# Kernel tuning notes

Measured on AMD Instinct MI355X. Metric: run time of the kernel, lower is better.

## Reference

```python
import jax, jax.numpy as jnp
import numpy as np

N_WIRES = 5
TOTAL = 2 * N_WIRES          # query branch simulates 2*n_wires qubits
DIM = 1 << TOTAL             # 1024
ENC = 1 << N_WIRES           # 32 = token encoder output dim


def setup_inputs() -> dict:
    key = jax.random.key(0)
    ks = jax.random.split(key, 6)
    B, T, C = 4, 32, 512
    x = jax.random.normal(ks[0], (B, T, C), jnp.float32)
    W_tok = jax.random.normal(ks[1], (ENC, C), jnp.float32) * 0.05
    b_tok = jax.random.normal(ks[2], (ENC,), jnp.float32) * 0.05
    theta_rx0 = jax.random.normal(ks[3], (TOTAL,), jnp.float32)
    theta_ry0 = jax.random.normal(ks[4], (TOTAL,), jnp.float32)
    theta_ry1 = jax.random.normal(ks[5], (TOTAL,), jnp.float32)
    return {"x": x, "W_tok": W_tok, "b_tok": b_tok,
            "theta_rx0": theta_rx0, "theta_ry0": theta_ry0, "theta_ry1": theta_ry1}


def _rx_mat(t):
    c = jnp.cos(t / 2).astype(jnp.complex64)
    s = jnp.sin(t / 2).astype(jnp.complex64)
    return jnp.stack([jnp.stack([c, -1j * s]), jnp.stack([-1j * s, c])])


def _ry_mat(t):
    c = jnp.cos(t / 2).astype(jnp.complex64)
    s = jnp.sin(t / 2).astype(jnp.complex64)
    return jnp.stack([jnp.stack([c, -s]), jnp.stack([s, c])])


def _apply_1q(state, U, w):
    # state: (bsz, 2, 2, ..., 2); wire w lives on axis 1+w (wire 0 = MSB)
    s = jnp.tensordot(state, U, axes=((1 + w,), (1,)))  # gate axis moves to last
    return jnp.moveaxis(s, -1, 1 + w)


def _apply_cnot(state, c, t):
    s = jnp.moveaxis(state, (1 + c, 1 + t), (-2, -1))
    s = s.at[..., 1, :].set(s[..., 1, ::-1])  # flip target where control == 1
    return jnp.moveaxis(s, (-2, -1), (1 + c, 1 + t))


def reference(x, W_tok, b_tok, theta_rx0, theta_ry0, theta_ry1):
    B, T, C = x.shape
    # token encoding + L2 normalize  -> (B, T, 32)
    enc = x @ W_tok.T + b_tok
    enc = enc / jnp.linalg.norm(enc, axis=-1, keepdims=True)
    # all T*T pairwise outer products, flattened as a_idx*32 + b_idx  -> (B, T*T, 1024)
    pairs = jnp.einsum('bip,bjq->bijpq', enc, enc).reshape(B, T * T, DIM)
    pairs = pairs / jnp.linalg.norm(pairs, axis=-1, keepdims=True)
    state = pairs.astype(jnp.complex64).reshape((B * T * T,) + (2,) * TOTAL)
    # layer 1: RX then RY on every wire
    for j in range(TOTAL):
        state = _apply_1q(state, _rx_mat(theta_rx0[j]), j)
        state = _apply_1q(state, _ry_mat(theta_ry0[j]), j)
    # CNOT ring
    for j in range(TOTAL):
        state = _apply_cnot(state, j, (j + 1) % TOTAL)
    # layer 2: RY on every wire
    for j in range(TOTAL):
        state = _apply_1q(state, _ry_mat(theta_ry1[j]), j)
    return state.reshape(B, T * T, DIM)
```

## Files before the change

### kernel.cpp

```cpp
#include <hip/hip_runtime.h>
#include <hip/hip_bf16.h>


__device__ __forceinline__ float2 shflx(float2 v, int mask) {
    return make_float2(__shfl_xor(v.x, mask, 64), __shfl_xor(v.y, mask, 64));
}

__global__ __launch_bounds__(256) void fused_kernel(const float* __restrict__ x,
                                                    const float* __restrict__ W,
                                                    const float* __restrict__ bt,
                                                    const float* __restrict__ rx0,
                                                    const float* __restrict__ ry0,
                                                    const float* __restrict__ ry1,
                                                    float* __restrict__ out,
                                                    int complex_out) {
    int bx = blockIdx.x;
    int b  = bx >> 8;
    int i  = (bx >> 3) & 31;
    int j0 = (bx & 7) * 4;
    int tid = threadIdx.x;

    __shared__ float g1[10][8];
    __shared__ float g2[10][2];
    __shared__ float esum[5][32];
    __shared__ float e[5][32];
    __shared__ float2 su[128];
    __shared__ float2 sv[4][128];

    if (tid < 10) {
        float sx, cx, s0, c0, s1, c1;
        sincosf(rx0[tid] * 0.5f, &sx, &cx);
        sincosf(ry0[tid] * 0.5f, &s0, &c0);
        sincosf(ry1[tid] * 0.5f, &s1, &c1);
        g1[tid][0] = c0 * cx;  g1[tid][1] = s0 * sx;
        g1[tid][2] = -s0 * cx; g1[tid][3] = -c0 * sx;
        g1[tid][4] = s0 * cx;  g1[tid][5] = -c0 * sx;
        g1[tid][6] = c0 * cx;  g1[tid][7] = -s0 * sx;
        g2[tid][0] = c1;       g2[tid][1] = s1;
    }

    {
        int col = tid >> 3;
        int kk  = tid & 7;
        const float4* wp = (const float4*)(W + (size_t)col * 512 + kk * 4);
        const float4* xp[5];
        xp[0] = (const float4*)(x + (size_t)(b * 32 + i) * 512 + kk * 4);
#pragma unroll
        for (int v = 1; v < 5; ++v)
            xp[v] = (const float4*)(x + (size_t)(b * 32 + j0 + v - 1) * 512 + kk * 4);
        float acc[5] = {0.f, 0.f, 0.f, 0.f, 0.f};
#pragma unroll
        for (int m = 0; m < 16; ++m) {
            float4 wv = wp[m * 8];
#pragma unroll
            for (int v = 0; v < 5; ++v) {
                float4 xv = xp[v][m * 8];
                acc[v] += xv.x * wv.x + xv.y * wv.y + xv.z * wv.z + xv.w * wv.w;
            }
        }
#pragma unroll
        for (int v = 0; v < 5; ++v) {
            acc[v] += __shfl_xor(acc[v], 1, 64);
            acc[v] += __shfl_xor(acc[v], 2, 64);
            acc[v] += __shfl_xor(acc[v], 4, 64);
        }
        if (kk == 0) {
#pragma unroll
            for (int v = 0; v < 5; ++v) esum[v][col] = acc[v];
        }
    }
    __syncthreads();

    if (tid < 160) {
        int v = tid >> 5, col = tid & 31;
        float sum = esum[v][col] + bt[col];
        float sq = sum * sum;
#pragma unroll
        for (int off = 1; off < 32; off <<= 1) sq += __shfl_xor(sq, off, 64);
        e[v][col] = sum * (1.0f / sqrtf(sq));
    }
    __syncthreads();

    {
        int grp = tid >> 5;
        int p = tid & 31;
#pragma unroll
        for (int it = 0; it < 3; ++it) {
            int job = it * 8 + grp;
            if (job < 20) {
                int v = job >> 2;
                int br = job & 3;
                int s = br >> 1, t = br & 1;
                int side = (v == 0) ? 0 : 1;
                int wb = side * 5;
                float2 c = make_float2(e[v][p], 0.f);
#pragma unroll
                for (int l = 0; l < 5; ++l) {
                    int w = wb + l, bit = 1 << (4 - l);
                    float2 pr = shflx(c, bit);
                    float a0 = g1[w][0], a1 = g1[w][1], a2 = g1[w][2], a3 = g1[w][3];
                    float a4 = g1[w][4], a5 = g1[w][5], a6 = g1[w][6], a7 = g1[w][7];
                    float2 lo, hi;
                    lo.x = a0 * c.x - a1 * c.y + a2 * pr.x - a3 * pr.y;
                    lo.y = a0 * c.y + a1 * c.x + a2 * pr.y + a3 * pr.x;
                    hi.x = a4 * pr.x - a5 * pr.y + a6 * c.x - a7 * c.y;
                    hi.y = a4 * pr.y + a5 * pr.x + a6 * c.y + a7 * c.x;
                    c = ((p & bit) == 0) ? lo : hi;
                }
                if (side == 0) {
#pragma unroll
                    for (int l = 0; l < 4; ++l) {
                        int cb = 1 << (4 - l), tb = 1 << (3 - l);
                        float2 pr = shflx(c, tb);
                        if (p & cb) c = pr;
                    }
                    if ((p & 1) != s) c = make_float2(0.f, 0.f);
                    { float2 pr = shflx(c, 16); if (t) c = pr; }
                } else {
                    { float2 pr = shflx(c, 16); if (s) c = pr; }
#pragma unroll
                    for (int l = 0; l < 4; ++l) {
                        int cb = 1 << (4 - l), tb = 1 << (3 - l);
                        float2 pr = shflx(c, tb);
                        if (p & cb) c = pr;
                    }
                    if ((p & 1) != t) c = make_float2(0.f, 0.f);
                }
#pragma unroll
                for (int l = 0; l < 5; ++l) {
                    int w = wb + l, bit = 1 << (4 - l);
                    float cy = g2[w][0], sy = g2[w][1];
                    float2 pr = shflx(c, bit);
                    c = ((p & bit) == 0)
                          ? make_float2(cy * c.x - sy * pr.x, cy * c.y - sy * pr.y)
                          : make_float2(sy * pr.x + cy * c.x, sy * pr.y + cy * c.y);
                }
                if (v == 0) su[br * 32 + p] = c;
                else        sv[v - 1][br * 32 + p] = c;
            }
        }
    }
    __syncthreads();

    int d0 = tid << 2;
    int pp = d0 >> 5;
    int q0 = d0 & 31;
    float2 up0 = su[pp], up1 = su[32 + pp], up2 = su[64 + pp], up3 = su[96 + pp];

#pragma unroll
    for (int jj = 0; jj < 4; ++jj) {
        const float2* svj = sv[jj];
        float2 acc[4];
#pragma unroll
        for (int ee = 0; ee < 4; ++ee) {
            int q = q0 + ee;
            float2 v0 = svj[q], v1 = svj[32 + q], v2 = svj[64 + q], v3 = svj[96 + q];
            float2 a;
            a.x = up0.x * v0.x - up0.y * v0.y + up1.x * v1.x - up1.y * v1.y
                + up2.x * v2.x - up2.y * v2.y + up3.x * v3.x - up3.y * v3.y;
            a.y = up0.x * v0.y + up0.y * v0.x + up1.x * v1.y + up1.y * v1.x
                + up2.x * v2.y + up2.y * v2.x + up3.x * v3.y + up3.y * v3.x;
            acc[ee] = a;
        }
        size_t pair = (size_t)b * 1024 + (size_t)i * 32 + (j0 + jj);
        if (complex_out) {
            float4* o = (float4*)(out + (pair * 1024 + d0) * 2);
            o[0] = make_float4(acc[0].x, acc[0].y, acc[1].x, acc[1].y);
            o[1] = make_float4(acc[2].x, acc[2].y, acc[3].x, acc[3].y);
        } else {
            float4* o = (float4*)(out + pair * 1024 + d0);
            o[0] = make_float4(acc[0].x, acc[1].x, acc[2].x, acc[3].x);
        }
    }
}

extern "C" void kernel_launch(void* const* d_in, const int* in_sizes, int n_in,
                              void* d_out, int out_size, void* d_ws, size_t ws_size,
                              hipStream_t stream) {
    const float* x   = (const float*)d_in[0];
    const float* W   = (const float*)d_in[1];
    const float* bt  = (const float*)d_in[2];
    const float* rx0 = (const float*)d_in[3];
    const float* ry0 = (const float*)d_in[4];
    const float* ry1 = (const float*)d_in[5];

    int complex_out = (out_size > 4 * 1024 * 1024) ? 1 : 0;
    fused_kernel<<<1024, 256, 0, stream>>>(x, W, bt, rx0, ry0, ry1,
                                           (float*)d_out, complex_out);
}
```

Before: 84.59 us.

## Split token encoding and per-token circuit into prep kernel, add nontemporal output stores

Moves the token encoder GEMV, normalization and the per-half circuit transforms into a separate prep kernel that runs once per token row (128 blocks). It writes U/V factor vectors to workspace, and the outer-product kernel then only loads them and writes the output. Before, each of the 1024 blocks recomputed five encodings and twenty circuit jobs, so this removes redundant compute. It also switches output writes to nontemporal stores. The cost is an extra kernel launch and a workspace round trip.

```diff
diff --git a/kernel.cpp b/kernel.cpp
--- a/kernel.cpp
+++ b/kernel.cpp
@@ -1,31 +1,28 @@
 #include <hip/hip_runtime.h>
 #include <hip/hip_bf16.h>
 
+
+typedef float vfloat4 __attribute__((ext_vector_type(4)));
 
 __device__ __forceinline__ float2 shflx(float2 v, int mask) {
     return make_float2(__shfl_xor(v.x, mask, 64), __shfl_xor(v.y, mask, 64));
 }
 
-__global__ __launch_bounds__(256) void fused_kernel(const float* __restrict__ x,
-                                                    const float* __restrict__ W,
-                                                    const float* __restrict__ bt,
-                                                    const float* __restrict__ rx0,
-                                                    const float* __restrict__ ry0,
-                                                    const float* __restrict__ ry1,
-                                                    float* __restrict__ out,
-                                                    int complex_out) {
-    int bx = blockIdx.x;
-    int b  = bx >> 8;
-    int i  = (bx >> 3) & 31;
-    int j0 = (bx & 7) * 4;
+__global__ __launch_bounds__(256) void prep_kernel(const float* __restrict__ x,
+                                                   const float* __restrict__ W,
+                                                   const float* __restrict__ bt,
+                                                   const float* __restrict__ rx0,
+                                                   const float* __restrict__ ry0,
+                                                   const float* __restrict__ ry1,
+                                                   float2* __restrict__ U,
+                                                   float2* __restrict__ V) {
+    int row = blockIdx.x;
     int tid = threadIdx.x;
 
     __shared__ float g1[10][8];
     __shared__ float g2[10][2];
-    __shared__ float esum[5][32];
-    __shared__ float e[5][32];
-    __shared__ float2 su[128];
-    __shared__ float2 sv[4][128];
+    __shared__ float esum[32];
+    __shared__ float e[32];
 
     if (tid < 10) {
         float sx, cx, s0, c0, s1, c1;
@@ -43,103 +40,100 @@
         int col = tid >> 3;
         int kk  = tid & 7;
         const float4* wp = (const float4*)(W + (size_t)col * 512 + kk * 4);
-        const float4* xp[5];
-        xp[0] = (const float4*)(x + (size_t)(b * 32 + i) * 512 + kk * 4);
-#pragma unroll
-        for (int v = 1; v < 5; ++v)
-            xp[v] = (const float4*)(x + (size_t)(b * 32 + j0 + v - 1) * 512 + kk * 4);
-        float acc[5] = {0.f, 0.f, 0.f, 0.f, 0.f};
+        const float4* xp = (const float4*)(x + (size_t)row * 512 + kk * 4);
+        float acc = 0.f;
 #pragma unroll
         for (int m = 0; m < 16; ++m) {
             float4 wv = wp[m * 8];
-#pragma unroll
-            for (int v = 0; v < 5; ++v) {
-                float4 xv = xp[v][m * 8];
-                acc[v] += xv.x * wv.x + xv.y * wv.y + xv.z * wv.z + xv.w * wv.w;
-            }
+            float4 xv = xp[m * 8];
+            acc += xv.x * wv.x + xv.y * wv.y + xv.z * wv.z + xv.w * wv.w;
         }
-#pragma unroll
-        for (int v = 0; v < 5; ++v) {
-            acc[v] += __shfl_xor(acc[v], 1, 64);
-            acc[v] += __shfl_xor(acc[v], 2, 64);
-            acc[v] += __shfl_xor(acc[v], 4, 64);
-        }
-        if (kk == 0) {
-#pragma unroll
-            for (int v = 0; v < 5; ++v) esum[v][col] = acc[v];
-        }
+        acc += __shfl_xor(acc, 1, 64);
+        acc += __shfl_xor(acc, 2, 64);
+        acc += __shfl_xor(acc, 4, 64);
+        if (kk == 0) esum[col] = acc;
     }
     __syncthreads();
 
-    if (tid < 160) {
-        int v = tid >> 5, col = tid & 31;
-        float sum = esum[v][col] + bt[col];
+    if (tid < 32) {
+        float sum = esum[tid] + bt[tid];
         float sq = sum * sum;
 #pragma unroll
         for (int off = 1; off < 32; off <<= 1) sq += __shfl_xor(sq, off, 64);
-        e[v][col] = sum * (1.0f / sqrtf(sq));
+        e[tid] = sum * (1.0f / sqrtf(sq));
     }
     __syncthreads();
 
     {
         int grp = tid >> 5;
+        int side = grp >> 2;
+        int br = grp & 3;
+        int s = br >> 1, t = br & 1;
         int p = tid & 31;
+        int wb = side * 5;
+        float2 c = make_float2(e[p], 0.f);
 #pragma unroll
-        for (int it = 0; it < 3; ++it) {
-            int job = it * 8 + grp;
-            if (job < 20) {
-                int v = job >> 2;
-                int br = job & 3;
-                int s = br >> 1, t = br & 1;
-                int side = (v == 0) ? 0 : 1;
-                int wb = side * 5;
-                float2 c = make_float2(e[v][p], 0.f);
+        for (int l = 0; l < 5; ++l) {
+            int w = wb + l, bit = 1 << (4 - l);
+            float2 pr = shflx(c, bit);
+            float a0 = g1[w][0], a1 = g1[w][1], a2 = g1[w][2], a3 = g1[w][3];
+            float a4 = g1[w][4], a5 = g1[w][5], a6 = g1[w][6], a7 = g1[w][7];
+            float2 lo, hi;
+            lo.x = a0 * c.x - a1 * c.y + a2 * pr.x - a3 * pr.y;
+            lo.y = a0 * c.y + a1 * c.x + a2 * pr.y + a3 * pr.x;
+            hi.x = a4 * pr.x - a5 * pr.y + a6 * c.x - a7 * c.y;
+            hi.y = a4 * pr.y + a5 * pr.x + a6 * c.y + a7 * c.x;
+            c = ((p & bit) == 0) ? lo : hi;
+        }
+        if (side == 0) {
 #pragma unroll
-                for (int l = 0; l < 5; ++l) {
-                    int w = wb + l, bit = 1 << (4 - l);
-                    float2 pr = shflx(c, bit);
-                    float a0 = g1[w][0], a1 = g1[w][1], a2 = g1[w][2], a3 = g1[w][3];
-                    float a4 = g1[w][4], a5 = g1[w][5], a6 = g1[w][6], a7 = g1[w][7];
-                    float2 lo, hi;
-                    lo.x = a0 * c.x - a1 * c.y + a2 * pr.x - a3 * pr.y;
-                    lo.y = a0 * c.y + a1 * c.x + a2 * pr.y + a3 * pr.x;
-                    hi.x = a4 * pr.x - a5 * pr.y + a6 * c.x - a7 * c.y;
-                    hi.y = a4 * pr.y + a5 * pr.x + a6 * c.y + a7 * c.x;
-                    c = ((p & bit) == 0) ? lo : hi;
-                }
-                if (side == 0) {
+            for (int l = 0; l < 4; ++l) {
+                int cb = 1 << (4 - l), tb = 1 << (3 - l);
+                float2 pr = shflx(c, tb);
+                if (p & cb) c = pr;
+            }
+            if ((p & 1) != s) c = make_float2(0.f, 0.f);
+            { float2 pr = shflx(c, 16); if (t) c = pr; }
+        } else {
+            { float2 pr = shflx(c, 16); if (s) c = pr; }
 #pragma unroll
-                    for (int l = 0; l < 4; ++l) {
-                        int cb = 1 << (4 - l), tb = 1 << (3 - l);
-                        float2 pr = shflx(c, tb);
-                        if (p & cb) c = pr;
-                    }
-                    if ((p & 1) != s) c = make_float2(0.f, 0.f);
-                    { float2 pr = shflx(c, 16); if (t) c = pr; }
-                } else {
-                    { float2 pr = shflx(c, 16); if (s) c = pr; }
+            for (int l = 0; l < 4; ++l) {
+                int cb = 1 << (4 - l), tb = 1 << (3 - l);
+                float2 pr = shflx(c, tb);
+                if (p & cb) c = pr;
+            }
+            if ((p & 1) != t) c = make_float2(0.f, 0.f);
+        }
 #pragma unroll
-                    for (int l = 0; l < 4; ++l) {
-                        int cb = 1 << (4 - l), tb = 1 << (3 - l);
-                        float2 pr = shflx(c, tb);
-                        if (p & cb) c = pr;
-                    }
-                    if ((p & 1) != t) c = make_float2(0.f, 0.f);
-                }
-#pragma unroll
-                for (int l = 0; l < 5; ++l) {
-                    int w = wb + l, bit = 1 << (4 - l);
-                    float cy = g2[w][0], sy = g2[w][1];
-                    float2 pr = shflx(c, bit);
-                    c = ((p & bit) == 0)
-                          ? make_float2(cy * c.x - sy * pr.x, cy * c.y - sy * pr.y)
-                          : make_float2(sy * pr.x + cy * c.x, sy * pr.y + cy * c.y);
-                }
-                if (v == 0) su[br * 32 + p] = c;
-                else        sv[v - 1][br * 32 + p] = c;
-            }
+        for (int l = 0; l < 5; ++l) {
+            int w = wb + l, bit = 1 << (4 - l);
+            float cy = g2[w][0], sy = g2[w][1];
+            float2 pr = shflx(c, bit);
+            c = ((p & bit) == 0)
+                  ? make_float2(cy * c.x - sy * pr.x, cy * c.y - sy * pr.y)
+                  : make_float2(sy * pr.x + cy * c.x, sy * pr.y + cy * c.y);
         }
+        float2* dst = (side == 0) ? U : V;
+        dst[(size_t)row * 128 + br * 32 + p] = c;
     }
+}
+
+__global__ __launch_bounds__(256) void outer_kernel(const float2* __restrict__ U,
+                                                    const float2* __restrict__ V,
+                                                    float* __restrict__ out,
+                                                    int complex_out) {
+    int bx = blockIdx.x;
+    int b  = bx >> 8;
+    int i  = (bx >> 3) & 31;
+    int j0 = (bx & 7) * 4;
+    int tid = threadIdx.x;
+
+    __shared__ float2 su[128];
+    __shared__ float2 sv[4][128];
+
+    if (tid < 64)
+        ((float4*)su)[tid] = ((const float4*)(U + (size_t)(b * 32 + i) * 128))[tid];
+    ((float4*)sv)[tid] = ((const float4*)(V + (size_t)(b * 32 + j0) * 128))[tid];
     __syncthreads();
 
     int d0 = tid << 2;
@@ -164,12 +158,15 @@
         }
         size_t pair = (size_t)b * 1024 + (size_t)i * 32 + (j0 + jj);
         if (complex_out) {
-            float4* o = (float4*)(out + (pair * 1024 + d0) * 2);
-            o[0] = make_float4(acc[0].x, acc[0].y, acc[1].x, acc[1].y);
-            o[1] = make_float4(acc[2].x, acc[2].y, acc[3].x, acc[3].y);
+            vfloat4* o = (vfloat4*)(out + (pair * 1024 + d0) * 2);
+            vfloat4 w0 = {acc[0].x, acc[0].y, acc[1].x, acc[1].y};
+            vfloat4 w1 = {acc[2].x, acc[2].y, acc[3].x, acc[3].y};
+            __builtin_nontemporal_store(w0, o);
+            __builtin_nontemporal_store(w1, o + 1);
         } else {
-            float4* o = (float4*)(out + pair * 1024 + d0);
-            o[0] = make_float4(acc[0].x, acc[1].x, acc[2].x, acc[3].x);
+            vfloat4* o = (vfloat4*)(out + pair * 1024 + d0);
+            vfloat4 w0 = {acc[0].x, acc[1].x, acc[2].x, acc[3].x};
+            __builtin_nontemporal_store(w0, o);
         }
     }
 }
@@ -184,7 +181,11 @@
     const float* ry0 = (const float*)d_in[4];
     const float* ry1 = (const float*)d_in[5];
 
+    float2* U = (float2*)d_ws;
+    float2* V = U + 16384;
+
+    prep_kernel<<<128, 256, 0, stream>>>(x, W, bt, rx0, ry0, ry1, U, V);
+
     int complex_out = (out_size > 4 * 1024 * 1024) ? 1 : 0;
-    fused_kernel<<<1024, 256, 0, stream>>>(x, W, bt, rx0, ry0, ry1,
-                                           (float*)d_out, complex_out);
+    outer_kernel<<<1024, 256, 0, stream>>>(U, V, (float*)d_out, complex_out);
 }
```

Result: faster. 74.97 us (-11.4%).
